# Kernel tuning notes

Measured on AMD Instinct MI355X. Metric: run time of the kernel, lower is better.

## Reference

```python
import jax, jax.numpy as jnp
import numpy as np
from jax import lax

D_STATE = 16
D_CONV = 4
DT_RANK = 64
D_INNER = 2048
D_MODEL = 1024


def setup_inputs() -> dict:
    key = jax.random.key(0)
    ks = jax.random.split(key, 12)
    B, L = 2, 1024
    s = lambda shape: 0.02
    inp = {
        "x": jax.random.normal(ks[0], (B, L, D_MODEL), jnp.float32),
        "in_proj_w": jax.random.normal(ks[1], (2 * D_INNER, D_MODEL), jnp.float32) * 0.02,
        "in_proj_b": jax.random.normal(ks[2], (2 * D_INNER,), jnp.float32) * 0.02,
        "conv_w": jax.random.normal(ks[3], (D_INNER, 1, D_CONV), jnp.float32) * 0.2,
        "conv_b": jax.random.normal(ks[4], (D_INNER,), jnp.float32) * 0.02,
        "x_proj_w": jax.random.normal(ks[5], (DT_RANK + 2 * D_STATE, D_INNER), jnp.float32) * 0.02,
        "dt_proj_w": jax.random.normal(ks[6], (D_INNER, DT_RANK), jnp.float32) * 0.02,
        "dt_proj_b": jax.random.normal(ks[7], (D_INNER,), jnp.float32) * 0.02,
        "A_log": jnp.log(jnp.tile(jnp.arange(1.0, D_STATE + 1.0, dtype=jnp.float32), (D_INNER, 1))),
        "D": jnp.ones((D_INNER,), jnp.float32),
        "out_proj_w": jax.random.normal(ks[8], (D_MODEL, D_INNER), jnp.float32) * 0.02,
        "out_proj_b": jax.random.normal(ks[9], (D_MODEL,), jnp.float32) * 0.02,
    }
    return inp


def _mamba_fwd(x, in_proj_w, in_proj_b, conv_w, conv_b, x_proj_w,
               dt_proj_w, dt_proj_b, A_log, D, out_proj_w, out_proj_b):
    Bsz, L, _ = x.shape
    # input projection -> two branches
    xz = x @ in_proj_w.T + in_proj_b                      # (B, L, 2*d_inner)
    x_branch, z_branch = jnp.split(xz, 2, axis=-1)        # (B, L, d_inner) each

    # causal depthwise conv over time (torch pads d_conv-1 both sides, slices to L == left-pad only)
    xc = x_branch.transpose(0, 2, 1)                      # (B, d_inner, L)
    xc = lax.conv_general_dilated(
        xc, conv_w,
        window_strides=(1,), padding=[(D_CONV - 1, 0)],
        dimension_numbers=("NCH", "OIH", "NCH"),
        feature_group_count=D_INNER,
    ) + conv_b[None, :, None]
    x_branch = jax.nn.silu(xc.transpose(0, 2, 1))         # (B, L, d_inner)
    z_branch = jax.nn.silu(z_branch)

    # data-dependent SSM parameters
    x_dbl = x_branch @ x_proj_w.T                         # (B, L, dt_rank + 2*d_state)
    dt, Bm, Cm = jnp.split(x_dbl, [DT_RANK, DT_RANK + D_STATE], axis=-1)
    dt = jax.nn.softplus(dt @ dt_proj_w.T + dt_proj_b)    # (B, L, d_inner)
    A = -jnp.exp(A_log)                                   # (d_inner, d_state)

    # selective scan over time
    def step(h, inputs):
        dt_t, B_t, C_t, x_t = inputs                      # (B,d_inner) (B,d_state) (B,d_state) (B,d_inner)
        dA = jnp.exp(dt_t[..., None] * A)                 # (B, d_inner, d_state)
        dB = dt_t[..., None] * B_t[:, None, :]            # (B, d_inner, d_state)
        h = dA * h + dB * x_t[..., None]
        y_t = jnp.einsum("bds,bs->bd", h, C_t)            # (B, d_inner)
        return h, y_t

    h0 = jnp.zeros((Bsz, D_INNER, D_STATE), x.dtype)
    xs = (dt.transpose(1, 0, 2), Bm.transpose(1, 0, 2), Cm.transpose(1, 0, 2), x_branch.transpose(1, 0, 2))
    _, y = lax.scan(step, h0, xs)                         # y: (L, B, d_inner)
    y = y.transpose(1, 0, 2)

    y = y + x_branch * D
    y = y * z_branch
    return y @ out_proj_w.T + out_proj_b                  # (B, L, d_model)


def reference(x, in_proj_w, in_proj_b, conv_w, conv_b, x_proj_w,
              dt_proj_w, dt_proj_b, A_log, D, out_proj_w, out_proj_b):
    return _mamba_fwd(x, in_proj_w, in_proj_b, conv_w, conv_b, x_proj_w,
                      dt_proj_w, dt_proj_b, A_log, D, out_proj_w, out_proj_b)
```

## Files before the change

### kernel.cpp

```cpp
#include <hip/hip_runtime.h>
#include <math.h>

#define D_STATE 16
#define D_CONV 4
#define DT_RANK 64
#define D_INNER 2048
#define D_MODEL 1024
#define BATCH 2
#define SEQLEN 1024
#define M_TOTAL (BATCH*SEQLEN)
#define REG ((size_t)M_TOTAL*D_INNER)

#define LC 64
#define NCHUNK (SEQLEN/LC)
#define CHB 64

#define XKSPLIT 16
#define XKCHUNK (D_INNER/XKSPLIT)
#define OSPLIT 4

typedef __fp16   h2s_t  __attribute__((ext_vector_type(2)));
typedef __fp16   h4s_t  __attribute__((ext_vector_type(4)));
typedef __fp16   h8s_t  __attribute__((ext_vector_type(8)));
typedef _Float16 half8  __attribute__((ext_vector_type(8)));
typedef float    floatx4 __attribute__((ext_vector_type(4)));

union HalfPack { h2s_t h2[4]; h8s_t h8; };

__device__ __forceinline__ float silu_f(float x) {
    return x / (1.0f + __expf(-x));
}
__device__ __forceinline__ float softplus_f(float x) {
    return fmaxf(x, 0.0f) + log1pf(__expf(-fabsf(x)));
}
__device__ __forceinline__ h8s_t pack8(const float4& v0, const float4& v1) {
    HalfPack p;
    p.h2[0] = __builtin_amdgcn_cvt_pkrtz(v0.x, v0.y);
    p.h2[1] = __builtin_amdgcn_cvt_pkrtz(v0.z, v0.w);
    p.h2[2] = __builtin_amdgcn_cvt_pkrtz(v1.x, v1.y);
    p.h2[3] = __builtin_amdgcn_cvt_pkrtz(v1.z, v1.w);
    return p.h8;
}
__device__ __forceinline__ void gll16(const __fp16* g, __fp16* l) {
    __builtin_amdgcn_global_load_lds(
        (__attribute__((address_space(1))) const void*)g,
        (__attribute__((address_space(3))) void*)l, 16, 0, 0);
}

#define N0 ((size_t)M_TOTAL*D_MODEL/8)
#define N1 ((size_t)2*D_INNER*D_MODEL/8)
#define N2 ((size_t)D_MODEL*D_INNER/8)
#define N3 ((size_t)96*D_INNER/8)
#define N4 ((size_t)D_INNER*DT_RANK/8)
#define NCVT (N0+N1+N2+N3+N4)

__global__ __launch_bounds__(256)
void cvt_all(const float* __restrict__ x,  const float* __restrict__ w1,
             const float* __restrict__ w2, const float* __restrict__ xpw,
             const float* __restrict__ dtw,
             __fp16* __restrict__ xh,  __fp16* __restrict__ wh1,
             __fp16* __restrict__ wh2, __fp16* __restrict__ xpwh,
             __fp16* __restrict__ dtwh)
{
    size_t i = (size_t)blockIdx.x * 256 + threadIdx.x;
    if (i >= NCVT) return;
    const float* src; __fp16* dst; size_t off;
    if      (i < N0)          { src = x;   dst = xh;   off = i; }
    else if (i < N0+N1)       { src = w1;  dst = wh1;  off = i - N0; }
    else if (i < N0+N1+N2)    { src = w2;  dst = wh2;  off = i - N0 - N1; }
    else if (i < N0+N1+N2+N3) { src = xpw; dst = xpwh; off = i - N0 - N1 - N2; }
    else                      { src = dtw; dst = dtwh; off = i - N0 - N1 - N2 - N3; }
    const float* p = src + off * 8;
    *(h8s_t*)(dst + off * 8) = pack8(*(const float4*)p, *(const float4*)(p + 4));
}

__global__ __launch_bounds__(256)
void out_init(float* __restrict__ out, const float* __restrict__ bias)
{
    size_t i = (size_t)blockIdx.x * 256 + threadIdx.x;
    int col = (int)((i * 4) & (D_MODEL - 1));
    *(float4*)(out + i * 4) = *(const float4*)(bias + col);
}

template<int MODE, int SPLITK>
__global__ __launch_bounds__(256)
void gemm_gll(const __fp16* __restrict__ A, int lda,
              const __fp16* __restrict__ B, int ldb,
              const float* __restrict__ bias,
              float* __restrict__ out0, __fp16* __restrict__ out1,
              int N, int K)
{
    constexpr int BM = 128, BN = 64, BK = 32;
    __shared__ __align__(16) __fp16 As[BM * BK];
    __shared__ __align__(16) __fp16 Bs[BN * BK];

    const int tid  = threadIdx.x;
    const int bm   = blockIdx.y * BM;
    const int bn   = blockIdx.x * BN;
    const int wave = tid >> 6;
    const int lane = tid & 63;
    const int wm   = wave * 32;
    const int fr   = lane & 15;
    const int fkh  = (lane >> 4) * 8;

    const int sr = tid >> 2;
    const int sc = (tid & 3) * 8;

    const int kspan = K / SPLITK;
    const int k0    = (SPLITK > 1) ? blockIdx.z * kspan : 0;

    const __fp16* gA0 = A + (size_t)(bm + sr) * lda + k0 + sc;
    const __fp16* gA1 = A + (size_t)(bm + sr + 64) * lda + k0 + sc;
    const __fp16* gB0 = B + (size_t)(bn + sr) * ldb + k0 + sc;
    __fp16* lA0 = &As[sr * BK + sc];
    __fp16* lA1 = &As[(sr + 64) * BK + sc];
    __fp16* lB0 = &Bs[sr * BK + sc];

    floatx4 zero = {0.f, 0.f, 0.f, 0.f};
    floatx4 acc[2][4];
    #pragma unroll
    for (int i = 0; i < 2; i++)
        #pragma unroll
        for (int j = 0; j < 4; j++) acc[i][j] = zero;

    for (int kt = 0; kt < kspan; kt += BK) {
        gll16(gA0 + kt, lA0);
        gll16(gA1 + kt, lA1);
        gll16(gB0 + kt, lB0);
        __syncthreads();

        half8 af[2], bf[4];
        #pragma unroll
        for (int i = 0; i < 2; i++)
            af[i] = *(half8*)&As[(wm + i*16 + fr) * BK + fkh];
        #pragma unroll
        for (int j = 0; j < 4; j++)
            bf[j] = *(half8*)&Bs[(j*16 + fr) * BK + fkh];
        #pragma unroll
        for (int i = 0; i < 2; i++)
            #pragma unroll
            for (int j = 0; j < 4; j++)
                acc[i][j] = __builtin_amdgcn_mfma_f32_16x16x32_f16(
                    af[i], bf[j], acc[i][j], 0, 0, 0);
        __syncthreads();
    }

    const int rbase = (lane >> 4) * 4;
    #pragma unroll
    for (int i = 0; i < 2; i++) {
        #pragma unroll
        for (int j = 0; j < 4; j++) {
            int n = bn + j*16 + fr;
            float bv = (MODE == 0) ? bias[n] : 0.0f;
            #pragma unroll
            for (int r = 0; r < 4; r++) {
                int m = bm + wm + i*16 + rbase + r;
                float v = acc[i][j][r] + bv;
                if (MODE == 0) {
                    if (n < D_INNER) out0[(size_t)m * D_INNER + n] = v;
                    else out1[(size_t)m * D_INNER + (n - D_INNER)] = (__fp16)silu_f(v);
                } else {
                    atomicAdd(out0 + (size_t)m * N + n, v);
                }
            }
        }
    }
}

__global__ __launch_bounds__(256)
void xproj_gll(const __fp16* __restrict__ A,
               const __fp16* __restrict__ B,
               float* __restrict__ partials)
{
    __shared__ __align__(16) __fp16 As[64 * 32];
    __shared__ __align__(16) __fp16 Bs[96 * 32];

    const int tid = threadIdx.x;
    const int mt  = blockIdx.x * 64;
    const int p   = blockIdx.y;
    const int k0  = p * XKCHUNK;
    const int wave = tid >> 6;
    const int lane = tid & 63;
    const int fr = lane & 15;
    const int fkh = (lane >> 4) * 8;

    floatx4 zero = {0.f, 0.f, 0.f, 0.f};
    floatx4 acc[6];
    #pragma unroll
    for (int j = 0; j < 6; j++) acc[j] = zero;

    for (int kt = 0; kt < XKCHUNK; kt += 32) {
        {
            int row = tid >> 2, col = (tid & 3) * 8;
            gll16(A + (size_t)(mt + row) * D_INNER + k0 + kt + col, &As[tid * 8]);
            gll16(B + (size_t)row * D_INNER + k0 + kt + col, &Bs[tid * 8]);
            if (tid < 128) {
                int c = tid + 256;
                gll16(B + (size_t)(c >> 2) * D_INNER + k0 + kt + (c & 3) * 8,
                      &Bs[c * 8]);
            }
        }
        __syncthreads();

        half8 af = *(half8*)&As[(wave * 16 + fr) * 32 + fkh];
        #pragma unroll
        for (int j = 0; j < 6; j++) {
            half8 bf = *(half8*)&Bs[(j * 16 + fr) * 32 + fkh];
            acc[j] = __builtin_amdgcn_mfma_f32_16x16x32_f16(af, bf, acc[j], 0, 0, 0);
        }
        __syncthreads();
    }

    const int rbase = (lane >> 4) * 4;
    float* outp = partials + ((size_t)p * M_TOTAL + mt + wave * 16) * 96;
    #pragma unroll
    for (int j = 0; j < 6; j++) {
        int n = j * 16 + fr;
        #pragma unroll
        for (int r = 0; r < 4; r++)
            outp[(size_t)(rbase + r) * 96 + n] = acc[j][r];
    }
}

__global__ __launch_bounds__(256)
void xproj_reduce(const float* __restrict__ partials,
                  float* __restrict__ xdbl, __fp16* __restrict__ dtrh)
{
    int i = blockIdx.x * 256 + threadIdx.x;
    float s = 0.0f;
    #pragma unroll
    for (int p = 0; p < XKSPLIT; p++)
        s += partials[(size_t)p * M_TOTAL * 96 + i];
    xdbl[i] = s;
    int col = i % 96;
    if (col < DT_RANK) dtrh[(size_t)(i / 96) * DT_RANK + col] = (__fp16)s;
}

__global__ __launch_bounds__(256)
void dtproj_mfma(const __fp16* __restrict__ A,
                 const __fp16* __restrict__ B,
                 const float* __restrict__ bias,
                 __fp16* __restrict__ dth)
{
    __shared__ __align__(16) __fp16 As[128 * 64];
    __shared__ __align__(16) __fp16 Bs[128 * 64];

    const int tid  = threadIdx.x;
    const int bm   = blockIdx.y * 128;
    const int bn   = blockIdx.x * 128;
    const int wave = tid >> 6;
    const int lane = tid & 63;
    const int wm   = (wave >> 1) * 64;
    const int wn   = (wave & 1) * 64;
    const int fr   = lane & 15;
    const int fkh  = (lane >> 4) * 8;

    #pragma unroll
    for (int r = 0; r < 4; r++) {
        int c = tid + 256 * r;
        int row = c >> 3, col = (c & 7) * 8;
        gll16(A + (size_t)(bm + row) * DT_RANK + col, &As[c * 8]);
        gll16(B + (size_t)(bn + row) * DT_RANK + col, &Bs[c * 8]);
    }
    __syncthreads();

    floatx4 zero = {0.f, 0.f, 0.f, 0.f};
    floatx4 acc[4][4];
    #pragma unroll
    for (int i = 0; i < 4; i++)
        #pragma unroll
        for (int j = 0; j < 4; j++) acc[i][j] = zero;

    #pragma unroll
    for (int ks = 0; ks < 64; ks += 32) {
        half8 af[4], bf[4];
        #pragma unroll
        for (int i = 0; i < 4; i++)
            af[i] = *(half8*)&As[(wm + i*16 + fr) * 64 + ks + fkh];
        #pragma unroll
        for (int j = 0; j < 4; j++)
            bf[j] = *(half8*)&Bs[(wn + j*16 + fr) * 64 + ks + fkh];
        #pragma unroll
        for (int i = 0; i < 4; i++)
            #pragma unroll
            for (int j = 0; j < 4; j++)
                acc[i][j] = __builtin_amdgcn_mfma_f32_16x16x32_f16(
                    af[i], bf[j], acc[i][j], 0, 0, 0);
    }

    const int rbase = (lane >> 4) * 4;
    #pragma unroll
    for (int i = 0; i < 4; i++) {
        #pragma unroll
        for (int j = 0; j < 4; j++) {
            int n = bn + wn + j*16 + fr;
            float bv = bias[n];
            #pragma unroll
            for (int r = 0; r < 4; r++) {
                int m = bm + wm + i*16 + rbase + r;
                dth[(size_t)m * D_INNER + n] = (__fp16)softplus_f(acc[i][j][r] + bv);
            }
        }
    }
}

__global__ __launch_bounds__(256)
void conv_silu_kernel(const float* __restrict__ xpre,
                      const float* __restrict__ conv_w,
                      const float* __restrict__ conv_b,
                      __fp16* __restrict__ xbh)
{
    int idx = blockIdx.x * blockDim.x + threadIdx.x;
    int c = idx % D_INNER;
    int l = (idx / D_INNER) % SEQLEN;
    int b = idx / (D_INNER * SEQLEN);
    const float* base = xpre + (size_t)b * SEQLEN * D_INNER + c;
    float w0 = conv_w[c*4+0], w1 = conv_w[c*4+1];
    float w2 = conv_w[c*4+2], w3 = conv_w[c*4+3];
    float acc = conv_b[c];
    if (l >= 3) acc += w0 * base[(l-3) * D_INNER];
    if (l >= 2) acc += w1 * base[(l-2) * D_INNER];
    if (l >= 1) acc += w2 * base[(l-1) * D_INNER];
    acc += w3 * base[l * D_INNER];
    xbh[idx] = (__fp16)silu_f(acc);
}

__global__ __launch_bounds__(256)
void scan_phase1(const __fp16* __restrict__ dth,
                 const float* __restrict__ xdbl,
                 const __fp16* __restrict__ xbh,
                 const float* __restrict__ A_log,
                 float* __restrict__ Pbuf, float* __restrict__ hbuf)
{
    int bx = blockIdx.x;
    int dg = bx & 31;
    int c  = (bx >> 5) & (NCHUNK - 1);
    int b  = bx >> 9;
    int d0 = dg * CHB;
    int t  = threadIdx.x;
    int s0 = (t & 3) * 4;
    int ch = t >> 2;
    int d  = d0 + ch;
    int l0 = c * LC;

    __shared__ __align__(16) float dt_t[LC][CHB];
    __shared__ __align__(16) float x_t[LC][CHB];
    __shared__ __align__(16) float B_t[LC][D_STATE];
    {
        int c4 = (t & 15) * 4;
        #pragma unroll
        for (int r = 0; r < 4; r++) {
            int row = (t >> 4) + r * 16;
            size_t g = (size_t)(b * SEQLEN + l0 + row) * D_INNER + d0 + c4;
            h4s_t d4 = *(const h4s_t*)(dth + g);
            h4s_t x4 = *(const h4s_t*)(xbh + g);
            float4 df = {(float)d4[0], (float)d4[1], (float)d4[2], (float)d4[3]};
            float4 xf = {(float)x4[0], (float)x4[1], (float)x4[2], (float)x4[3]};
            *(float4*)&dt_t[row][c4] = df;
            *(float4*)&x_t[row][c4]  = xf;
        }
        int brow = t >> 2, bc4 = (t & 3) * 4;
        *(float4*)&B_t[brow][bc4] =
            *(const float4*)(xdbl + (size_t)(b*SEQLEN + l0 + brow)*96 + DT_RANK + bc4);
    }
    float4 Al = *(const float4*)(A_log + d * D_STATE + s0);
    float As0 = -__expf(Al.x), As1 = -__expf(Al.y);
    float As2 = -__expf(Al.z), As3 = -__expf(Al.w);
    __syncthreads();

    float h0=0,h1=0,h2=0,h3=0, P0=1,P1=1,P2=1,P3=1;
    #pragma unroll 4
    for (int l = 0; l < LC; l++) {
        float dtv = dt_t[l][ch];
        float dx  = dtv * x_t[l][ch];
        float4 Bv = *(float4*)&B_t[l][s0];
        float a0 = __expf(dtv*As0), a1 = __expf(dtv*As1);
        float a2 = __expf(dtv*As2), a3 = __expf(dtv*As3);
        h0 = a0*h0 + dx*Bv.x;  P0 *= a0;
        h1 = a1*h1 + dx*Bv.y;  P1 *= a1;
        h2 = a2*h2 + dx*Bv.z;  P2 *= a2;
        h3 = a3*h3 + dx*Bv.w;  P3 *= a3;
    }
    size_t idx = (((size_t)(b * NCHUNK + c)) * D_INNER + d) * D_STATE + s0;
    float4 Pv = {P0,P1,P2,P3}, hv = {h0,h1,h2,h3};
    *(float4*)&Pbuf[idx] = Pv;
    *(float4*)&hbuf[idx] = hv;
}

__global__ __launch_bounds__(256)
void scan_carry(float* __restrict__ Pbuf, const float* __restrict__ hbuf)
{
    int t = blockIdx.x * 256 + threadIdx.x;
    int s0 = (t & 3) * 4;
    int bd = t >> 2;
    int d = bd & (D_INNER - 1);
    int b = bd >> 11;
    float4 h = {0,0,0,0};
    #pragma unroll
    for (int c = 0; c < NCHUNK; c++) {
        size_t idx = (((size_t)(b * NCHUNK + c)) * D_INNER + d) * D_STATE + s0;
        float4 Pc = *(float4*)&Pbuf[idx];
        float4 hl = *(const float4*)&hbuf[idx];
        *(float4*)&Pbuf[idx] = h;
        h.x = Pc.x*h.x + hl.x;  h.y = Pc.y*h.y + hl.y;
        h.z = Pc.z*h.z + hl.z;  h.w = Pc.w*h.w + hl.w;
    }
}

__global__ __launch_bounds__(256)
void scan_phase2(const __fp16* __restrict__ dth,
                 const float* __restrict__ xdbl,
                 const __fp16* __restrict__ xbh,
                 const float* __restrict__ A_log,
                 const float* __restrict__ Dvec,
                 const float* __restrict__ hinbuf,
                 const __fp16* __restrict__ zh,
                 __fp16* __restrict__ yh)
{
    int bx = blockIdx.x;
    int dg = bx & 31;
    int c  = (bx >> 5) & (NCHUNK - 1);
    int b  = bx >> 9;
    int d0 = dg * CHB;
    int t  = threadIdx.x;
    int s0 = (t & 3) * 4;
    int ch = t >> 2;
    int d  = d0 + ch;
    int l0 = c * LC;

    __shared__ __align__(16) float dt_t[LC][CHB];
    __shared__ __align__(16) float x_t[LC][CHB];
    __shared__ __align__(16) float B_t[LC][D_STATE];
    __shared__ __align__(16) float C_t[LC][D_STATE];
    __shared__ __align__(16) float y_t[LC][CHB];
    {
        int c4 = (t & 15) * 4;
        #pragma unroll
        for (int r = 0; r < 4; r++) {
            int row = (t >> 4) + r * 16;
            size_t g = (size_t)(b * SEQLEN + l0 + row) * D_INNER + d0 + c4;
            h4s_t d4 = *(const h4s_t*)(dth + g);
            h4s_t x4 = *(const h4s_t*)(xbh + g);
            float4 df = {(float)d4[0], (float)d4[1], (float)d4[2], (float)d4[3]};
            float4 xf = {(float)x4[0], (float)x4[1], (float)x4[2], (float)x4[3]};
            *(float4*)&dt_t[row][c4] = df;
            *(float4*)&x_t[row][c4]  = xf;
        }
        int brow = t >> 2, bc4 = (t & 3) * 4;
        const float* bcbase = xdbl + (size_t)(b*SEQLEN + l0 + brow)*96 + DT_RANK + bc4;
        *(float4*)&B_t[brow][bc4] = *(const float4*)bcbase;
        *(float4*)&C_t[brow][bc4] = *(const float4*)(bcbase + D_STATE);
    }
    float4 Al = *(const float4*)(A_log + d * D_STATE + s0);
    float As0 = -__expf(Al.x), As1 = -__expf(Al.y);
    float As2 = -__expf(Al.z), As3 = -__expf(Al.w);
    float Dd = Dvec[d];
    size_t idx = (((size_t)(b * NCHUNK + c)) * D_INNER + d) * D_STATE + s0;
    float4 hv = *(const float4*)&hinbuf[idx];
    float h0 = hv.x, h1 = hv.y, h2 = hv.z, h3 = hv.w;
    __syncthreads();

    #pragma unroll 4
    for (int l = 0; l < LC; l++) {
        float dtv = dt_t[l][ch];
        float xv  = x_t[l][ch];
        float dx  = dtv * xv;
        float4 Bv = *(float4*)&B_t[l][s0];
        float4 Cv = *(float4*)&C_t[l][s0];
        float a0 = __expf(dtv*As0), a1 = __expf(dtv*As1);
        float a2 = __expf(dtv*As2), a3 = __expf(dtv*As3);
        h0 = a0*h0 + dx*Bv.x;
        h1 = a1*h1 + dx*Bv.y;
        h2 = a2*h2 + dx*Bv.z;
        h3 = a3*h3 + dx*Bv.w;
        float p = h0*Cv.x + h1*Cv.y + h2*Cv.z + h3*Cv.w;
        p += __shfl_xor(p, 1);
        p += __shfl_xor(p, 2);
        if ((t & 3) == 0) y_t[l][ch] = p + xv * Dd;
    }
    __syncthreads();
    {
        int c4 = (t & 15) * 4;
        #pragma unroll
        for (int r = 0; r < 4; r++) {
            int row = (t >> 4) + r * 16;
            size_t g = (size_t)(b * SEQLEN + l0 + row) * D_INNER + d0 + c4;
            float4 y4 = *(float4*)&y_t[row][c4];
            h4s_t z4 = *(const h4s_t*)(zh + g);
            h4s_t o;
            o[0] = (__fp16)(y4.x * (float)z4[0]);
            o[1] = (__fp16)(y4.y * (float)z4[1]);
            o[2] = (__fp16)(y4.z * (float)z4[2]);
            o[3] = (__fp16)(y4.w * (float)z4[3]);
            *(h4s_t*)(yh + g) = o;
        }
    }
}

extern "C" void kernel_launch(void* const* d_in, const int* in_sizes, int n_in,
                              void* d_out, int out_size, void* d_ws, size_t ws_size,
                              hipStream_t stream)
{
    const float* x          = (const float*)d_in[0];
    const float* in_proj_w  = (const float*)d_in[1];
    const float* in_proj_b  = (const float*)d_in[2];
    const float* conv_w     = (const float*)d_in[3];
    const float* conv_b     = (const float*)d_in[4];
    const float* x_proj_w   = (const float*)d_in[5];
    const float* dt_proj_w  = (const float*)d_in[6];
    const float* dt_proj_b  = (const float*)d_in[7];
    const float* A_log      = (const float*)d_in[8];
    const float* Dv         = (const float*)d_in[9];
    const float* out_proj_w = (const float*)d_in[10];
    const float* out_proj_b = (const float*)d_in[11];
    float* out = (float*)d_out;

    char* base = (char*)d_ws;
    float*  xpre  = (float*) (base + 0);
    __fp16* zh    = (__fp16*)(base + 16777216);
    __fp16* yh    = (__fp16*)(base + 25165824);
    __fp16* xbh   = (__fp16*)(base + 33554432);
    __fp16* xh    = (__fp16*)(base + 41943040);
    __fp16* wh1   = (__fp16*)(base + 46137344);
    __fp16* wh2   = (__fp16*)(base + 54525952);
    __fp16* xpwh  = (__fp16*)(base + 58720256);
    __fp16* dtwh  = (__fp16*)(base + 59113472);
    float*  xdbl  = (float*) (base + 59375616);
    __fp16* dtrh  = (__fp16*)(base + 60162048);
    __fp16* dth   = (__fp16*)(base + 60424192);
    float*  xpart = (float*) (base + 68812800);
    float*  Pbuf  = (float*) (base + 81395712);
    float*  hbuf  = (float*) (base + 85590016);

    cvt_all<<<(NCVT + 255) / 256, 256, 0, stream>>>(
        x, in_proj_w, out_proj_w, x_proj_w, dt_proj_w,
        xh, wh1, wh2, xpwh, dtwh);

    {
        dim3 grid((2*D_INNER)/64, M_TOTAL/128, 1);
        gemm_gll<0,1><<<grid, 256, 0, stream>>>(
            xh, D_MODEL, wh1, D_MODEL, in_proj_b,
            xpre, zh, 2*D_INNER, D_MODEL);
    }
    conv_silu_kernel<<<(BATCH*SEQLEN*D_INNER)/256, 256, 0, stream>>>(
        xpre, conv_w, conv_b, xbh);
    {
        dim3 grid(M_TOTAL/64, XKSPLIT);
        xproj_gll<<<grid, 256, 0, stream>>>(xbh, xpwh, xpart);
        xproj_reduce<<<(M_TOTAL*96)/256, 256, 0, stream>>>(xpart, xdbl, dtrh);
    }
    {
        dim3 grid(D_INNER/128, M_TOTAL/128);
        dtproj_mfma<<<grid, 256, 0, stream>>>(dtrh, dtwh, dt_proj_b, dth);
    }
    {
        int nblk = BATCH * NCHUNK * (D_INNER / CHB);
        scan_phase1<<<nblk, 256, 0, stream>>>(dth, xdbl, xbh, A_log, Pbuf, hbuf);
        scan_carry<<<(BATCH*D_INNER*4)/256, 256, 0, stream>>>(Pbuf, hbuf);
        scan_phase2<<<nblk, 256, 0, stream>>>(dth, xdbl, xbh, A_log, Dv, Pbuf, zh, yh);
    }
    out_init<<<(M_TOTAL*D_MODEL/4)/256, 256, 0, stream>>>(out, out_proj_b);
    {
        dim3 grid(D_MODEL/64, M_TOTAL/128, OSPLIT);
        gemm_gll<1,OSPLIT><<<grid, 256, 0, stream>>>(
            yh, D_INNER, wh2, D_INNER, nullptr,
            out, nullptr, D_MODEL, D_INNER);
    }
}
```

Before: 260.5 us.

## Rework GEMM to register-loaded A with double-buffered swizzled B, fp16 conv input

The GEMM kernel now loads A fragments straight from global memory into registers. B is staged through a double-buffered, XOR-swizzled LDS tile with BK=64, so the next tile's load overlaps the current MFMA work. The in_proj output for the x branch is stored as fp16 instead of fp32, which halves that traffic, and the conv kernel is vectorised to handle 4 channels per thread on fp16 input. The output bias initialisation is folded into the conversion kernel, removing one launch. Storing the pre-conv activation in fp16 adds rounding error, and uncached direct A loads could raise global memory traffic.

```diff
diff --git a/kernel.cpp b/kernel.cpp
--- a/kernel.cpp
+++ b/kernel.cpp
@@ -52,18 +52,26 @@
 #define N2 ((size_t)D_MODEL*D_INNER/8)
 #define N3 ((size_t)96*D_INNER/8)
 #define N4 ((size_t)D_INNER*DT_RANK/8)
-#define NCVT (N0+N1+N2+N3+N4)
+#define N5 ((size_t)M_TOTAL*D_MODEL/8)
+#define NCVT (N0+N1+N2+N3+N4+N5)
 
 __global__ __launch_bounds__(256)
 void cvt_all(const float* __restrict__ x,  const float* __restrict__ w1,
              const float* __restrict__ w2, const float* __restrict__ xpw,
-             const float* __restrict__ dtw,
+             const float* __restrict__ dtw, const float* __restrict__ obias,
              __fp16* __restrict__ xh,  __fp16* __restrict__ wh1,
              __fp16* __restrict__ wh2, __fp16* __restrict__ xpwh,
-             __fp16* __restrict__ dtwh)
+             __fp16* __restrict__ dtwh, float* __restrict__ out)
 {
     size_t i = (size_t)blockIdx.x * 256 + threadIdx.x;
     if (i >= NCVT) return;
+    if (i >= N0+N1+N2+N3+N4) {
+        size_t off = i - (N0+N1+N2+N3+N4);
+        int col = (int)((off * 8) & (D_MODEL - 1));
+        *(float4*)(out + off * 8)     = *(const float4*)(obias + col);
+        *(float4*)(out + off * 8 + 4) = *(const float4*)(obias + col + 4);
+        return;
+    }
     const float* src; __fp16* dst; size_t off;
     if      (i < N0)          { src = x;   dst = xh;   off = i; }
     else if (i < N0+N1)       { src = w1;  dst = wh1;  off = i - N0; }
@@ -74,47 +82,37 @@
     *(h8s_t*)(dst + off * 8) = pack8(*(const float4*)p, *(const float4*)(p + 4));
 }
 
-__global__ __launch_bounds__(256)
-void out_init(float* __restrict__ out, const float* __restrict__ bias)
-{
-    size_t i = (size_t)blockIdx.x * 256 + threadIdx.x;
-    int col = (int)((i * 4) & (D_MODEL - 1));
-    *(float4*)(out + i * 4) = *(const float4*)(bias + col);
-}
-
 template<int MODE, int SPLITK>
 __global__ __launch_bounds__(256)
-void gemm_gll(const __fp16* __restrict__ A, int lda,
-              const __fp16* __restrict__ B, int ldb,
-              const float* __restrict__ bias,
-              float* __restrict__ out0, __fp16* __restrict__ out1,
-              int N, int K)
-{
-    constexpr int BM = 128, BN = 64, BK = 32;
-    __shared__ __align__(16) __fp16 As[BM * BK];
-    __shared__ __align__(16) __fp16 Bs[BN * BK];
+void gemm_ra(const __fp16* __restrict__ A, int lda,
+             const __fp16* __restrict__ B, int ldb,
+             const float* __restrict__ bias,
+             float* __restrict__ outf,
+             __fp16* __restrict__ outh0, __fp16* __restrict__ outh1,
+             int N, int K)
+{
+    constexpr int BK = 64;
+    __shared__ __align__(16) __fp16 Bs[2][64 * BK];
 
     const int tid  = threadIdx.x;
-    const int bm   = blockIdx.y * BM;
-    const int bn   = blockIdx.x * BN;
+    const int bm   = blockIdx.y * 128;
+    const int bn   = blockIdx.x * 64;
     const int wave = tid >> 6;
     const int lane = tid & 63;
-    const int wm   = wave * 32;
     const int fr   = lane & 15;
-    const int fkh  = (lane >> 4) * 8;
-
-    const int sr = tid >> 2;
-    const int sc = (tid & 3) * 8;
+    const int g    = lane >> 4;
 
     const int kspan = K / SPLITK;
     const int k0    = (SPLITK > 1) ? blockIdx.z * kspan : 0;
-
-    const __fp16* gA0 = A + (size_t)(bm + sr) * lda + k0 + sc;
-    const __fp16* gA1 = A + (size_t)(bm + sr + 64) * lda + k0 + sc;
-    const __fp16* gB0 = B + (size_t)(bn + sr) * ldb + k0 + sc;
-    __fp16* lA0 = &As[sr * BK + sc];
-    __fp16* lA1 = &As[(sr + 64) * BK + sc];
-    __fp16* lB0 = &Bs[sr * BK + sc];
+    const int NIT   = kspan / BK;
+
+    const int c0 = tid,        r0 = c0 >> 3, s0 = (c0 & 7) ^ (r0 & 7);
+    const int c1 = tid + 256,  r1 = c1 >> 3, s1 = (c1 & 7) ^ (r1 & 7);
+    const __fp16* gB0 = B + (size_t)(bn + r0) * ldb + k0 + s0 * 8;
+    const __fp16* gB1 = B + (size_t)(bn + r1) * ldb + k0 + s1 * 8;
+
+    const __fp16* pA0 = A + (size_t)(bm + wave*32 + fr) * lda + k0 + g * 8;
+    const __fp16* pA1 = pA0 + (size_t)16 * lda;
 
     floatx4 zero = {0.f, 0.f, 0.f, 0.f};
     floatx4 acc[2][4];
@@ -123,29 +121,32 @@
         #pragma unroll
         for (int j = 0; j < 4; j++) acc[i][j] = zero;
 
-    for (int kt = 0; kt < kspan; kt += BK) {
-        gll16(gA0 + kt, lA0);
-        gll16(gA1 + kt, lA1);
-        gll16(gB0 + kt, lB0);
+    gll16(gB0, &Bs[0][c0 * 8]);
+    gll16(gB1, &Bs[0][c1 * 8]);
+
+    for (int kt = 0; kt < NIT; kt++) {
         __syncthreads();
-
-        half8 af[2], bf[4];
-        #pragma unroll
-        for (int i = 0; i < 2; i++)
-            af[i] = *(half8*)&As[(wm + i*16 + fr) * BK + fkh];
-        #pragma unroll
-        for (int j = 0; j < 4; j++)
-            bf[j] = *(half8*)&Bs[(j*16 + fr) * BK + fkh];
-        #pragma unroll
-        for (int i = 0; i < 2; i++)
+        if (kt + 1 < NIT) {
+            gll16(gB0 + (kt+1) * BK, &Bs[(kt+1) & 1][c0 * 8]);
+            gll16(gB1 + (kt+1) * BK, &Bs[(kt+1) & 1][c1 * 8]);
+        }
+        const __fp16* bufp = Bs[kt & 1];
+        #pragma unroll
+        for (int ks = 0; ks < 2; ks++) {
+            half8 a0 = *(const half8*)(pA0 + kt * BK + ks * 32);
+            half8 a1 = *(const half8*)(pA1 + kt * BK + ks * 32);
             #pragma unroll
-            for (int j = 0; j < 4; j++)
-                acc[i][j] = __builtin_amdgcn_mfma_f32_16x16x32_f16(
-                    af[i], bf[j], acc[i][j], 0, 0, 0);
-        __syncthreads();
-    }
-
-    const int rbase = (lane >> 4) * 4;
+            for (int j = 0; j < 4; j++) {
+                int prow = j * 16 + fr;
+                int pchk = prow * 8 + (((ks << 2) | g) ^ (prow & 7));
+                half8 bf = *(const half8*)&bufp[pchk * 8];
+                acc[0][j] = __builtin_amdgcn_mfma_f32_16x16x32_f16(a0, bf, acc[0][j], 0, 0, 0);
+                acc[1][j] = __builtin_amdgcn_mfma_f32_16x16x32_f16(a1, bf, acc[1][j], 0, 0, 0);
+            }
+        }
+    }
+
+    const int rbase = g * 4;
     #pragma unroll
     for (int i = 0; i < 2; i++) {
         #pragma unroll
@@ -154,13 +155,13 @@
             float bv = (MODE == 0) ? bias[n] : 0.0f;
             #pragma unroll
             for (int r = 0; r < 4; r++) {
-                int m = bm + wm + i*16 + rbase + r;
+                int m = bm + wave*32 + i*16 + rbase + r;
                 float v = acc[i][j][r] + bv;
                 if (MODE == 0) {
-                    if (n < D_INNER) out0[(size_t)m * D_INNER + n] = v;
-                    else out1[(size_t)m * D_INNER + (n - D_INNER)] = (__fp16)silu_f(v);
+                    if (n < D_INNER) outh0[(size_t)m * D_INNER + n] = (__fp16)v;
+                    else outh1[(size_t)m * D_INNER + (n - D_INNER)] = (__fp16)silu_f(v);
                 } else {
-                    atomicAdd(out0 + (size_t)m * N + n, v);
+                    atomicAdd(outf + (size_t)m * N + n, v);
                 }
             }
         }
@@ -305,24 +306,37 @@
 }
 
 __global__ __launch_bounds__(256)
-void conv_silu_kernel(const float* __restrict__ xpre,
+void conv_silu_kernel(const __fp16* __restrict__ xpreh,
                       const float* __restrict__ conv_w,
                       const float* __restrict__ conv_b,
                       __fp16* __restrict__ xbh)
 {
     int idx = blockIdx.x * blockDim.x + threadIdx.x;
-    int c = idx % D_INNER;
-    int l = (idx / D_INNER) % SEQLEN;
-    int b = idx / (D_INNER * SEQLEN);
-    const float* base = xpre + (size_t)b * SEQLEN * D_INNER + c;
-    float w0 = conv_w[c*4+0], w1 = conv_w[c*4+1];
-    float w2 = conv_w[c*4+2], w3 = conv_w[c*4+3];
-    float acc = conv_b[c];
-    if (l >= 3) acc += w0 * base[(l-3) * D_INNER];
-    if (l >= 2) acc += w1 * base[(l-2) * D_INNER];
-    if (l >= 1) acc += w2 * base[(l-1) * D_INNER];
-    acc += w3 * base[l * D_INNER];
-    xbh[idx] = (__fp16)silu_f(acc);
+    int cq = idx & (D_INNER/4 - 1);
+    int l  = (idx / (D_INNER/4)) & (SEQLEN - 1);
+    int b  = idx / (D_INNER/4 * SEQLEN);
+    int c  = cq * 4;
+    const __fp16* base = xpreh + (size_t)b * SEQLEN * D_INNER + c;
+    float4 w0 = *(const float4*)(conv_w + c*4);
+    float4 w1 = *(const float4*)(conv_w + (c+1)*4);
+    float4 w2 = *(const float4*)(conv_w + (c+2)*4);
+    float4 w3 = *(const float4*)(conv_w + (c+3)*4);
+    float4 bv = *(const float4*)(conv_b + c);
+    float a0 = bv.x, a1 = bv.y, a2 = bv.z, a3 = bv.w;
+    #pragma unroll
+    for (int k = 0; k < 4; k++) {
+        int ls = l - (3 - k);
+        if (ls < 0) continue;
+        h4s_t v = *(const h4s_t*)(base + (size_t)ls * D_INNER);
+        a0 += ((const float*)&w0)[k] * (float)v[0];
+        a1 += ((const float*)&w1)[k] * (float)v[1];
+        a2 += ((const float*)&w2)[k] * (float)v[2];
+        a3 += ((const float*)&w3)[k] * (float)v[3];
+    }
+    h4s_t o;
+    o[0] = (__fp16)silu_f(a0); o[1] = (__fp16)silu_f(a1);
+    o[2] = (__fp16)silu_f(a2); o[3] = (__fp16)silu_f(a3);
+    *(h4s_t*)(xbh + (size_t)b * SEQLEN * D_INNER + (size_t)l * D_INNER + c) = o;
 }
 
 __global__ __launch_bounds__(256)
@@ -516,7 +530,7 @@
     float* out = (float*)d_out;
 
     char* base = (char*)d_ws;
-    float*  xpre  = (float*) (base + 0);
+    __fp16* xpreh = (__fp16*)(base + 0);
     __fp16* zh    = (__fp16*)(base + 16777216);
     __fp16* yh    = (__fp16*)(base + 25165824);
     __fp16* xbh   = (__fp16*)(base + 33554432);
@@ -533,17 +547,17 @@
     float*  hbuf  = (float*) (base + 85590016);
 
     cvt_all<<<(NCVT + 255) / 256, 256, 0, stream>>>(
-        x, in_proj_w, out_proj_w, x_proj_w, dt_proj_w,
-        xh, wh1, wh2, xpwh, dtwh);
+        x, in_proj_w, out_proj_w, x_proj_w, dt_proj_w, out_proj_b,
+        xh, wh1, wh2, xpwh, dtwh, out);
 
     {
         dim3 grid((2*D_INNER)/64, M_TOTAL/128, 1);
-        gemm_gll<0,1><<<grid, 256, 0, stream>>>(
+        gemm_ra<0,1><<<grid, 256, 0, stream>>>(
             xh, D_MODEL, wh1, D_MODEL, in_proj_b,
-            xpre, zh, 2*D_INNER, D_MODEL);
-    }
-    conv_silu_kernel<<<(BATCH*SEQLEN*D_INNER)/256, 256, 0, stream>>>(
-        xpre, conv_w, conv_b, xbh);
+            nullptr, xpreh, zh, 2*D_INNER, D_MODEL);
+    }
+    conv_silu_kernel<<<(BATCH*SEQLEN*D_INNER/4)/256, 256, 0, stream>>>(
+        xpreh, conv_w, conv_b, xbh);
     {
         dim3 grid(M_TOTAL/64, XKSPLIT);
         xproj_gll<<<grid, 256, 0, stream>>>(xbh, xpwh, xpart);
@@ -559,11 +573,10 @@
         scan_carry<<<(BATCH*D_INNER*4)/256, 256, 0, stream>>>(Pbuf, hbuf);
         scan_phase2<<<nblk, 256, 0, stream>>>(dth, xdbl, xbh, A_log, Dv, Pbuf, zh, yh);
     }
-    out_init<<<(M_TOTAL*D_MODEL/4)/256, 256, 0, stream>>>(out, out_proj_b);
     {
         dim3 grid(D_MODEL/64, M_TOTAL/128, OSPLIT);
-        gemm_gll<1,OSPLIT><<<grid, 256, 0, stream>>>(
+        gemm_ra<1,OSPLIT><<<grid, 256, 0, stream>>>(
             yh, D_INNER, wh2, D_INNER, nullptr,
-            out, nullptr, D_MODEL, D_INNER);
-    }
-}
+            out, nullptr, nullptr, D_MODEL, D_INNER);
+    }
+}
```

After: 277.8 us. 6.6% more time.
